# Optimization experiments

Hardware: AMD Instinct MI355X
Metric: run time of the kernel (lower is better)

Reference implementation:

```python
import jax, jax.numpy as jnp
import numpy as np

EPS = 1e-5
D_MODEL, N_HEADS, D_FF, SEQ, BATCH, THETA = 1024, 16, 4096, 2048, 4, 10000.0


def rmsnorm(x, g):
    rms = jnp.sqrt(jnp.mean(jnp.square(x), axis=-1, keepdims=True) + EPS)
    return (x / rms) * g


def rope(x, pos, theta):
    # x: [B, H, S, Dh]; pos: [S]
    dh = x.shape[-1]
    inv_freq = theta ** (-jnp.arange(0, dh, 2, dtype=x.dtype) / dh)  # [Dh/2]
    ang = pos.astype(x.dtype)[:, None] * inv_freq                    # [S, Dh/2]
    cos, sin = jnp.cos(ang), jnp.sin(ang)
    x1, x2 = x[..., ::2], x[..., 1::2]
    r1 = x1 * cos - x2 * sin
    r2 = x1 * sin + x2 * cos
    return jnp.stack([r1, r2], axis=-1).reshape(x.shape)


def setup_inputs() -> dict:
    key = jax.random.key(0)
    ks = jax.random.split(key, 10)
    s = 0.02
    return {
        "x": jax.random.normal(ks[0], (BATCH, SEQ, D_MODEL), jnp.float32),
        "token_positions": jnp.arange(SEQ, dtype=jnp.int64 if jax.config.x64_enabled else jnp.int32),
        "g1": jnp.ones((D_MODEL,), jnp.float32),
        "g2": jnp.ones((D_MODEL,), jnp.float32),
        "wq": jax.random.normal(ks[1], (D_MODEL, D_MODEL), jnp.float32) * s,
        "wk": jax.random.normal(ks[2], (D_MODEL, D_MODEL), jnp.float32) * s,
        "wv": jax.random.normal(ks[3], (D_MODEL, D_MODEL), jnp.float32) * s,
        "wo": jax.random.normal(ks[4], (D_MODEL, D_MODEL), jnp.float32) * s,
        "w1": jax.random.normal(ks[5], (D_MODEL, D_FF), jnp.float32) * s,
        "w2": jax.random.normal(ks[6], (D_FF, D_MODEL), jnp.float32) * s,
        "w3": jax.random.normal(ks[7], (D_MODEL, D_FF), jnp.float32) * s,
    }


def reference(x, token_positions, g1, g2, wq, wk, wv, wo, w1, w2, w3):
    B, S, D = x.shape
    H = N_HEADS
    Dh = D // H

    # --- RMSNorm 1 + causal RoPE self-attention ---
    h = rmsnorm(x, g1)
    q = (h @ wq).reshape(B, S, H, Dh).transpose(0, 2, 1, 3)  # [B,H,S,Dh]
    k = (h @ wk).reshape(B, S, H, Dh).transpose(0, 2, 1, 3)
    v = (h @ wv).reshape(B, S, H, Dh).transpose(0, 2, 1, 3)
    q = rope(q, token_positions, THETA)
    k = rope(k, token_positions, THETA)

    scores = jnp.einsum("bhqd,bhkd->bhqk", q, k) / jnp.sqrt(jnp.asarray(Dh, x.dtype))
    causal = jnp.tril(jnp.ones((S, S), bool))
    scores = jnp.where(causal, scores, jnp.asarray(-jnp.inf, x.dtype))
    attn = jax.nn.softmax(scores, axis=-1)
    ctx = jnp.einsum("bhqk,bhkd->bhqd", attn, v)             # [B,H,S,Dh]
    ctx = ctx.transpose(0, 2, 1, 3).reshape(B, S, D)
    attn_out = ctx @ wo

    y = x + attn_out  # residual

    # --- RMSNorm 2 + SwiGLU ---
    h2 = rmsnorm(y, g2)
    gate = jax.nn.silu(h2 @ w1) * (h2 @ w3)
    ff = gate @ w2

    return y + ff
```

## Files before the change

kernel.cpp:

```cpp
#include <hip/hip_runtime.h>
#include <hip/hip_bf16.h>
#include <cstdint>
#include <cstddef>

typedef __bf16 bf16_t;
typedef __bf16 bf16x8 __attribute__((ext_vector_type(8)));
typedef __bf16 bf16x4 __attribute__((ext_vector_type(4)));
typedef float  f32x4  __attribute__((ext_vector_type(4)));

#define D_MODEL 1024
#define SEQ     2048
#define NHEADS  16
#define DHEAD   64
#define DFF     4096

__device__ __forceinline__ void async_ld16(void* lds, const void* g) {
    __builtin_amdgcn_global_load_lds(
        (__attribute__((address_space(1))) void*)(void*)(g),
        (__attribute__((address_space(3))) void*)(lds), 16, 0, 0);
}

__device__ __forceinline__ void xcd_swizzle(int& bx, int& by) {
    const int gy = gridDim.y;
    const int i = blockIdx.x + gridDim.x * blockIdx.y;
    if ((gy & 7) == 0) {
        const int cy = gy >> 3;
        const int xcd = i & 7, j = i >> 3;
        bx = j / cy;
        by = xcd * cy + (j % cy);
    } else { bx = blockIdx.x; by = blockIdx.y; }
}

__global__ __launch_bounds__(256)
void transpose_cast_kernel(const float* __restrict__ src, bf16_t* __restrict__ dst,
                           int K, int N, int gstride, int goff)
{
    __shared__ float tile[32][33];
    const int bn = blockIdx.x * 32, bk = blockIdx.y * 32;
    const int tx = threadIdx.x & 31, ty = threadIdx.x >> 5;
#pragma unroll
    for (int i = 0; i < 32; i += 8)
        tile[ty + i][tx] = src[(size_t)(bk + ty + i) * N + bn + tx];
    __syncthreads();
#pragma unroll
    for (int i = 0; i < 32; i += 8) {
        const int n = bn + ty + i, kk = bk + tx;
        const int row = (n >> 4) * gstride + (n & 15) + goff;
        dst[(size_t)row * K + kk] = (bf16_t)tile[tx][ty + i];
    }
}

__global__ __launch_bounds__(256)
void transpose_v_kernel(const bf16_t* __restrict__ v, bf16_t* __restrict__ vt)
{
    __shared__ bf16_t T[64 * 66];
    const int bh = blockIdx.y, s0 = blockIdx.x * 64;
    const int tid = threadIdx.x;
    const size_t vb = (size_t)bh * SEQ * DHEAD;
#pragma unroll
    for (int h = 0; h < 2; ++h) {
        const int s = h * 32 + (tid >> 3), dc = (tid & 7) * 8;
        const bf16x8 vv = *(const bf16x8*)(v + vb + (size_t)(s0 + s) * DHEAD + dc);
#pragma unroll
        for (int j = 0; j < 8; ++j) T[(dc + j) * 66 + s] = vv[j];
    }
    __syncthreads();
    const size_t tb = (size_t)bh * DHEAD * SEQ;
    const uint32_t* Tw = (const uint32_t*)T;
#pragma unroll
    for (int h = 0; h < 2; ++h) {
        const int dh = h * 32 + (tid >> 3), kc = (tid & 7) * 8;
        uint4 o;
        o.x = Tw[dh * 33 + kc / 2 + 0];
        o.y = Tw[dh * 33 + kc / 2 + 1];
        o.z = Tw[dh * 33 + kc / 2 + 2];
        o.w = Tw[dh * 33 + kc / 2 + 3];
        *(uint4*)(vt + tb + (size_t)dh * SEQ + s0 + kc) = o;
    }
}

__global__ __launch_bounds__(256)
void rmsnorm_kernel(const float* __restrict__ x, const float* __restrict__ gw,
                    bf16_t* __restrict__ out)
{
    const int row = blockIdx.x, tid = threadIdx.x;
    const float4 v = ((const float4*)(x + (size_t)row * D_MODEL))[tid];
    float ss = v.x*v.x + v.y*v.y + v.z*v.z + v.w*v.w;
#pragma unroll
    for (int d = 1; d < 64; d <<= 1) ss += __shfl_xor(ss, d);
    __shared__ float red[4];
    if ((tid & 63) == 0) red[tid >> 6] = ss;
    __syncthreads();
    const float tot = red[0] + red[1] + red[2] + red[3];
    const float sc = rsqrtf(tot * (1.f / D_MODEL) + 1e-5f);
    const float4 gv = ((const float4*)gw)[tid];
    bf16x4 o;
    o[0] = (bf16_t)(v.x * sc * gv.x);
    o[1] = (bf16_t)(v.y * sc * gv.y);
    o[2] = (bf16_t)(v.z * sc * gv.z);
    o[3] = (bf16_t)(v.w * sc * gv.w);
    ((bf16x4*)(out + (size_t)row * D_MODEL))[tid] = o;
}

template <int MODE>
__global__ __launch_bounds__(512, 2)
void gemm256_kernel(const bf16_t* __restrict__ A, const bf16_t* __restrict__ Bt,
                    int M, int N, int K,
                    bf16_t* __restrict__ qo, bf16_t* __restrict__ ko, bf16_t* __restrict__ vo,
                    bf16_t* __restrict__ gate)
{
    __shared__ bf16x8 lds[8192];
    const int tid  = threadIdx.x;
    const int wave = tid >> 6;
    const int lane = tid & 63;
    const int r = lane & 15, g = lane >> 4;
    const int wm = wave >> 2;
    const int wn = wave & 3;
    const int r3 = (r >> 3) & 1;
    const int gx = g ^ (((r >> 2) & 1) << 1);
    const int cx0 = r3 * 4 + gx;
    const int cx1 = cx0 ^ 4;

    int bx, by;
    xcd_swizzle(bx, by);
    const int row0 = by * 256;
    const int col0 = bx * 256;

    const f32x4 fzero = {0.f, 0.f, 0.f, 0.f};
    f32x4 acc[8][4];
#pragma unroll
    for (int i = 0; i < 8; ++i)
#pragma unroll
        for (int j = 0; j < 4; ++j) acc[i][j] = fzero;

    const int kcx = ((tid & 7) ^ (((tid >> 5) & 1) << 1) ^ (((tid >> 6) & 1) << 2)) * 8;
    const bf16_t* aSrc = A  + (size_t)(row0 + (tid >> 3)) * K + kcx;
    const bf16_t* bSrc = Bt + (size_t)(col0 + (tid >> 3)) * K + kcx;

    const int aRB = wm * 1024 + r * 8;
    const int bRB = 2048 + (wn >> 1) * 1024 + ((wn & 1) * 64 + r) * 8;

#define STA(nb, ktn, h_, j_) \
    async_ld16(&lds[(nb) + (h_) * 1024 + (j_) * 512 + tid], \
               aSrc + (size_t)((h_) * 128 + (j_) * 64) * K + (ktn))
#define STB(nb, ktn, h_, j_) \
    async_ld16(&lds[(nb) + 2048 + (h_) * 1024 + (j_) * 512 + tid], \
               bSrc + (size_t)((h_) * 128 + (j_) * 64) * K + (ktn))

    STB(0, 0, 0, 0); STB(0, 0, 0, 1); STB(0, 0, 1, 0); STB(0, 0, 1, 1);
    STA(0, 0, 0, 0); STA(0, 0, 1, 0);
    STA(0, 0, 0, 1); STA(0, 0, 1, 1);
    asm volatile("s_waitcnt vmcnt(2)" ::: "memory");
    __builtin_amdgcn_s_barrier();

    bf16x8 aF[8], bF[8];

    const int NT = K >> 6;
    for (int t = 0; t < NT; ++t) {
        const int AB  = (t & 1) << 12;
        const int nb  = AB ^ 4096;
        const int ktn = (t + 1) << 6;
        const bool pf = (t + 1) < NT;

#pragma unroll
        for (int q = 0; q < 4; ++q) {
            aF[q * 2 + 0] = lds[AB + aRB + q * 128 + cx0];
            aF[q * 2 + 1] = lds[AB + aRB + q * 128 + cx1];
        }
#pragma unroll
        for (int n = 0; n < 2; ++n) {
            bF[n * 2 + 0] = lds[AB + bRB + n * 128 + cx0];
            bF[n * 2 + 1] = lds[AB + bRB + n * 128 + cx1];
        }
        if (pf) { STB(nb, ktn, 0, 0); STB(nb, ktn, 0, 1); }
        __builtin_amdgcn_s_barrier();
        asm volatile("s_waitcnt lgkmcnt(0)" ::: "memory");
        __builtin_amdgcn_sched_barrier(0);
        __builtin_amdgcn_s_setprio(1);
#pragma unroll
        for (int q = 0; q < 4; ++q)
#pragma unroll
            for (int n = 0; n < 2; ++n)
#pragma unroll
                for (int ks = 0; ks < 2; ++ks)
                    acc[q][n] = __builtin_amdgcn_mfma_f32_16x16x32_bf16(
                        aF[q * 2 + ks], bF[n * 2 + ks], acc[q][n], 0, 0, 0);
        __builtin_amdgcn_s_setprio(0);
        __builtin_amdgcn_s_barrier();

#pragma unroll
        for (int n = 0; n < 2; ++n) {
            bF[4 + n * 2 + 0] = lds[AB + bRB + (32 + n * 16) * 8 + cx0];
            bF[4 + n * 2 + 1] = lds[AB + bRB + (32 + n * 16) * 8 + cx1];
        }
        if (pf) { STB(nb, ktn, 1, 0); STB(nb, ktn, 1, 1); }
        __builtin_amdgcn_s_barrier();
        asm volatile("s_waitcnt lgkmcnt(0)" ::: "memory");
        __builtin_amdgcn_sched_barrier(0);
        __builtin_amdgcn_s_setprio(1);
#pragma unroll
        for (int q = 0; q < 4; ++q)
#pragma unroll
            for (int n = 0; n < 2; ++n)
#pragma unroll
                for (int ks = 0; ks < 2; ++ks)
                    acc[q][2 + n] = __builtin_amdgcn_mfma_f32_16x16x32_bf16(
                        aF[q * 2 + ks], bF[4 + n * 2 + ks], acc[q][2 + n], 0, 0, 0);
        __builtin_amdgcn_s_setprio(0);
        if (pf) asm volatile("s_waitcnt vmcnt(4)" ::: "memory");
        else    asm volatile("s_waitcnt vmcnt(0)" ::: "memory");
        __builtin_amdgcn_s_barrier();

#pragma unroll
        for (int q = 0; q < 4; ++q) {
            aF[q * 2 + 0] = lds[AB + aRB + (64 + q * 16) * 8 + cx0];
            aF[q * 2 + 1] = lds[AB + aRB + (64 + q * 16) * 8 + cx1];
        }
        if (pf) { STA(nb, ktn, 0, 0); STA(nb, ktn, 1, 0); }
        __builtin_amdgcn_s_barrier();
        asm volatile("s_waitcnt lgkmcnt(0)" ::: "memory");
        __builtin_amdgcn_sched_barrier(0);
        __builtin_amdgcn_s_setprio(1);
#pragma unroll
        for (int q = 0; q < 4; ++q)
#pragma unroll
            for (int n = 0; n < 2; ++n)
#pragma unroll
                for (int ks = 0; ks < 2; ++ks)
                    acc[4 + q][2 + n] = __builtin_amdgcn_mfma_f32_16x16x32_bf16(
                        aF[q * 2 + ks], bF[4 + n * 2 + ks], acc[4 + q][2 + n], 0, 0, 0);
        __builtin_amdgcn_s_setprio(0);
        __builtin_amdgcn_s_barrier();

        if (pf) { STA(nb, ktn, 0, 1); STA(nb, ktn, 1, 1); }
        __builtin_amdgcn_s_barrier();
        __builtin_amdgcn_s_setprio(1);
#pragma unroll
        for (int q = 0; q < 4; ++q)
#pragma unroll
            for (int n = 0; n < 2; ++n)
#pragma unroll
                for (int ks = 0; ks < 2; ++ks)
                    acc[4 + q][n] = __builtin_amdgcn_mfma_f32_16x16x32_bf16(
                        aF[q * 2 + ks], bF[n * 2 + ks], acc[4 + q][n], 0, 0, 0);
        __builtin_amdgcn_s_setprio(0);
        if (pf) asm volatile("s_waitcnt vmcnt(2)" ::: "memory");
        __builtin_amdgcn_s_barrier();
    }
#undef STA
#undef STB

    const int mbase = row0 + wm * 128 + g * 4;
    const int nbase = col0 + wn * 64 + r;

    if constexpr (MODE == 2) {
#pragma unroll
        for (int np = 0; np < 2; ++np) {
            const int gc = (col0 >> 1) + wn * 32 + np * 16 + r;
#pragma unroll
            for (int mt = 0; mt < 8; ++mt) {
#pragma unroll
                for (int e = 0; e < 4; ++e) {
                    const float v1 = acc[mt][2 * np][e];
                    const float v3 = acc[mt][2 * np + 1][e];
                    const float sv = v1 * __builtin_amdgcn_rcpf(1.f + __expf(-v1));
                    const int grow = mbase + mt * 16 + e;
                    gate[(size_t)grow * DFF + gc] = (bf16_t)(sv * v3);
                }
            }
        }
    } else {
#pragma unroll
        for (int nt = 0; nt < 4; ++nt) {
            const int gcol = nbase + nt * 16;
            const int mat  = gcol >> 10;
            const int d    = gcol & 1023;
            const int head = d >> 6;
            const int dh   = d & 63;
            const float invf = __expf((float)(dh & ~1) * -0.14391157f);
            const size_t hb = (size_t)head * SEQ * DHEAD + dh;
#pragma unroll
            for (int mt = 0; mt < 8; ++mt) {
#pragma unroll
                for (int e = 0; e < 4; ++e) {
                    const float val = acc[mt][nt][e];
                    const float partner = __shfl_xor(val, 1);
                    const int grow = mbase + mt * 16 + e;
                    const int b = grow >> 11;
                    const int s = grow & 2047;
                    const size_t dst = (size_t)b * NHEADS * SEQ * DHEAD + hb + (size_t)s * DHEAD;
                    if (mat == 2) {
                        vo[dst] = (bf16_t)val;
                    } else {
                        float sn, cs;
                        __sincosf((float)s * invf, &sn, &cs);
                        const float rv = (dh & 1) ? (partner * sn + val * cs)
                                                  : (val * cs - partner * sn);
                        if (mat == 0) qo[dst] = (bf16_t)(rv * 0.125f);
                        else          ko[dst] = (bf16_t)rv;
                    }
                }
            }
        }
    }
}

template <int MODE>
__global__ __launch_bounds__(256, 3)
void gemm128_kernel(const bf16_t* __restrict__ A, const bf16_t* __restrict__ Bt,
                    int M, int N, int K, const float* res, float* outf)
{
    __shared__ bf16x8 Al[1024];
    __shared__ bf16x8 Bl[1024];
    const int tid  = threadIdx.x;
    const int wave = tid >> 6;
    const int lane = tid & 63;
    const int r    = lane & 15;
    const int g    = lane >> 4;
    const int wm   = wave >> 1;
    const int wn   = wave & 1;
    const int r3 = (r >> 3) & 1;
    const int gx = g ^ (((r >> 2) & 1) << 1);
    const int cx0 = r3 * 4 + gx;
    const int cx1 = cx0 ^ 4;

    int bx, by;
    xcd_swizzle(bx, by);
    const int row0 = by * 128;
    const int col0 = bx * 128;

    const f32x4 fzero = {0.f, 0.f, 0.f, 0.f};
    f32x4 acc[4][4];
#pragma unroll
    for (int i = 0; i < 4; ++i)
#pragma unroll
        for (int j = 0; j < 4; ++j) acc[i][j] = fzero;

    const int kcx = ((tid & 7) ^ (((tid >> 5) & 1) << 1) ^ (((tid >> 6) & 1) << 2)) * 8;
    const bf16_t* a0 = A  + (size_t)(row0 + (tid >> 3)) * K + kcx;
    const bf16_t* b0 = Bt + (size_t)(col0 + (tid >> 3)) * K + kcx;

    for (int kt = 0; kt < K; kt += 64) {
#pragma unroll
        for (int j = 0; j < 4; ++j)
            async_ld16(&Al[j * 256 + tid], a0 + kt + (size_t)(j * 32) * K);
#pragma unroll
        for (int j = 0; j < 4; ++j)
            async_ld16(&Bl[j * 256 + tid], b0 + kt + (size_t)(j * 32) * K);
        __syncthreads();
#pragma unroll
        for (int s = 0; s < 2; ++s) {
            const int cx = s ? cx1 : cx0;
            bf16x8 af[4], bfr[4];
#pragma unroll
            for (int mt = 0; mt < 4; ++mt) af[mt]  = Al[(wm * 64 + mt * 16 + r) * 8 + cx];
#pragma unroll
            for (int nt = 0; nt < 4; ++nt) bfr[nt] = Bl[(wn * 64 + nt * 16 + r) * 8 + cx];
#pragma unroll
            for (int mt = 0; mt < 4; ++mt)
#pragma unroll
                for (int nt = 0; nt < 4; ++nt)
                    acc[mt][nt] = __builtin_amdgcn_mfma_f32_16x16x32_bf16(
                        af[mt], bfr[nt], acc[mt][nt], 0, 0, 0);
        }
        __syncthreads();
    }

    const int mbase = row0 + wm * 64 + g * 4;
    const int nbase = col0 + wn * 64 + r;
#pragma unroll
    for (int mt = 0; mt < 4; ++mt) {
#pragma unroll
        for (int nt = 0; nt < 4; ++nt) {
#pragma unroll
            for (int e = 0; e < 4; ++e) {
                const int grow = mbase + mt * 16 + e;
                const int gcol = nbase + nt * 16;
                const size_t idx = (size_t)grow * D_MODEL + gcol;
                outf[idx] = res[idx] + acc[mt][nt][e];
            }
        }
    }
}

__global__ __launch_bounds__(256)
void attn_kernel(const bf16_t* __restrict__ qg, const bf16_t* __restrict__ kg,
                 const bf16_t* __restrict__ vT, bf16_t* __restrict__ ctx)
{
    __shared__ bf16x8 lds[4096];
    const int qblk = (gridDim.x - 1) - blockIdx.x;
    const int bh   = blockIdx.y;
    const int tid  = threadIdx.x;
    const int wave = tid >> 6;
    const int lane = tid & 63;
    const int r = lane & 15, g = lane >> 4;
    const size_t base = (size_t)bh * SEQ * DHEAD;
    const int qw = qblk * 128 + wave * 32;

    bf16x8 qf[2][2];
#pragma unroll
    for (int rt = 0; rt < 2; ++rt)
#pragma unroll
        for (int kh = 0; kh < 2; ++kh)
            qf[rt][kh] = *(const bf16x8*)(qg + base + (size_t)(qw + rt*16 + r) * DHEAD + kh*32 + g*8);

    const f32x4 fzero = {0.f, 0.f, 0.f, 0.f};
    f32x4 O[2][4];
    float mi[2][4], li[2][4];
#pragma unroll
    for (int rt = 0; rt < 2; ++rt)
#pragma unroll
        for (int e = 0; e < 4; ++e) { mi[rt][e] = -1e30f; li[rt][e] = 0.f; }
#pragma unroll
    for (int rt = 0; rt < 2; ++rt)
#pragma unroll
        for (int d = 0; d < 4; ++d) O[rt][d] = fzero;

    bf16_t* const Pb = (bf16_t*)&lds[2048 + wave * 512];

    for (int kb = 0; kb <= qblk; ++kb) {
        const int k0 = kb * 128;
        {
            const int ghalf = (wave >> 1);
            const int key   = (wave & 1) * 64 + lane;
            const bf16_t* kp = kg + base + (size_t)(k0 + key) * DHEAD + ghalf * 8;
#pragma unroll
            for (int i = 0; i < 4; ++i)
                async_ld16(&lds[i * 256 + wave * 64], kp + i * 16);
        }
        {
            const bf16_t* vp = vT + base + (size_t)lane * SEQ + k0 + wave * 8;
#pragma unroll
            for (int i = 0; i < 4; ++i)
                async_ld16(&lds[1024 + i * 256 + wave * 64], vp + i * 32);
        }
        __syncthreads();

        f32x4 sc[2][8];
        __builtin_amdgcn_s_setprio(1);
#pragma unroll
        for (int ct = 0; ct < 8; ++ct) {
            const bf16x8 kf0 = lds[g * 128 + ct * 16 + r];
            const bf16x8 kf1 = lds[(4 + g) * 128 + ct * 16 + r];
            sc[0][ct] = __builtin_amdgcn_mfma_f32_16x16x32_bf16(qf[0][0], kf0, fzero, 0, 0, 0);
            sc[0][ct] = __builtin_amdgcn_mfma_f32_16x16x32_bf16(qf[0][1], kf1, sc[0][ct], 0, 0, 0);
            sc[1][ct] = __builtin_amdgcn_mfma_f32_16x16x32_bf16(qf[1][0], kf0, fzero, 0, 0, 0);
            sc[1][ct] = __builtin_amdgcn_mfma_f32_16x16x32_bf16(qf[1][1], kf1, sc[1][ct], 0, 0, 0);
        }
        __builtin_amdgcn_s_setprio(0);
        if (kb == qblk) {
#pragma unroll
            for (int rt = 0; rt < 2; ++rt)
#pragma unroll
                for (int ct = 0; ct < 8; ++ct)
#pragma unroll
                    for (int e = 0; e < 4; ++e)
                        if (ct * 16 + r > wave * 32 + rt * 16 + g * 4 + e)
                            sc[rt][ct][e] = -1e30f;
        }
#pragma unroll
        for (int rt = 0; rt < 2; ++rt) {
#pragma unroll
            for (int e = 0; e < 4; ++e) {
                float mx = sc[rt][0][e];
#pragma unroll
                for (int ct = 1; ct < 8; ++ct) mx = fmaxf(mx, sc[rt][ct][e]);
#pragma unroll
                for (int d = 1; d < 16; d <<= 1) mx = fmaxf(mx, __shfl_xor(mx, d));
                const float mnew  = fmaxf(mi[rt][e], mx);
                const float alpha = __expf(mi[rt][e] - mnew);
                mi[rt][e] = mnew;
                float pv[8], rs = 0.f;
#pragma unroll
                for (int ct = 0; ct < 8; ++ct) { pv[ct] = __expf(sc[rt][ct][e] - mnew); rs += pv[ct]; }
#pragma unroll
                for (int d = 1; d < 16; d <<= 1) rs += __shfl_xor(rs, d);
                li[rt][e] = li[rt][e] * alpha + rs;
#pragma unroll
                for (int dht = 0; dht < 4; ++dht) O[rt][dht][e] *= alpha;
                const int qlocal = rt * 16 + g * 4 + e;
#pragma unroll
                for (int ct = 0; ct < 8; ++ct) {
                    const int kchunk = ct * 2 + (r >> 3);
                    Pb[(kchunk * 32 + qlocal) * 8 + (r & 7)] = (bf16_t)pv[ct];
                }
            }
        }
        __builtin_amdgcn_s_setprio(1);
#pragma unroll
        for (int kt = 0; kt < 4; ++kt) {
            const bf16x8 pf0 = lds[2048 + wave * 512 + (kt * 4 + g) * 32 + r];
            const bf16x8 pf1 = lds[2048 + wave * 512 + (kt * 4 + g) * 32 + 16 + r];
#pragma unroll
            for (int dht = 0; dht < 4; ++dht) {
                const bf16x8 vf = lds[1024 + (kt * 4 + g) * 64 + dht * 16 + r];
                O[0][dht] = __builtin_amdgcn_mfma_f32_16x16x32_bf16(pf0, vf, O[0][dht], 0, 0, 0);
                O[1][dht] = __builtin_amdgcn_mfma_f32_16x16x32_bf16(pf1, vf, O[1][dht], 0, 0, 0);
            }
        }
        __builtin_amdgcn_s_setprio(0);
        __syncthreads();
    }

    const int b = bh >> 4, head = bh & 15;
#pragma unroll
    for (int rt = 0; rt < 2; ++rt) {
#pragma unroll
        for (int e = 0; e < 4; ++e) {
            const float inv = __builtin_amdgcn_rcpf(li[rt][e]);
            const int s = qw + rt * 16 + g * 4 + e;
            bf16_t* op = ctx + ((size_t)(b * SEQ + s)) * D_MODEL + head * DHEAD + r;
#pragma unroll
            for (int dht = 0; dht < 4; ++dht)
                op[dht * 16] = (bf16_t)(O[rt][dht][e] * inv);
        }
    }
}

extern "C" void kernel_launch(void* const* d_in, const int* in_sizes, int n_in,
                              void* d_out, int out_size, void* d_ws, size_t ws_size,
                              hipStream_t stream)
{
    (void)in_sizes; (void)n_in; (void)out_size; (void)ws_size;
    const float* x  = (const float*)d_in[0];
    const float* g1 = (const float*)d_in[2];
    const float* g2 = (const float*)d_in[3];
    const float* wq = (const float*)d_in[4];
    const float* wk = (const float*)d_in[5];
    const float* wv = (const float*)d_in[6];
    const float* wo = (const float*)d_in[7];
    const float* w1 = (const float*)d_in[8];
    const float* w2 = (const float*)d_in[9];
    const float* w3 = (const float*)d_in[10];
    float* out = (float*)d_out;
    char* ws = (char*)d_ws;
    const size_t MB = 1ull << 20;
    bf16_t* wqkvT = (bf16_t*)(ws + 0);
    bf16_t* woT   = (bf16_t*)(ws + 6  * MB);
    bf16_t* w13T  = (bf16_t*)(ws + 8  * MB);
    bf16_t* w2T   = (bf16_t*)(ws + 24 * MB);
    bf16_t* hbuf  = (bf16_t*)(ws + 32 * MB);
    bf16_t* qbuf  = (bf16_t*)(ws + 48 * MB);
    bf16_t* kbuf  = (bf16_t*)(ws + 64 * MB);
    bf16_t* vbuf  = (bf16_t*)(ws + 80 * MB);
    bf16_t* ctx   = (bf16_t*)(ws + 96 * MB);
    bf16_t* gate  = (bf16_t*)(ws + 48 * MB);
    bf16_t* vTb   = hbuf;

    dim3 blk(256);
    dim3 blk5(512);
    transpose_cast_kernel<<<dim3(32, 32),  blk, 0, stream>>>(wq, wqkvT,             1024, 1024, 16, 0);
    transpose_cast_kernel<<<dim3(32, 32),  blk, 0, stream>>>(wk, wqkvT + 1024*1024, 1024, 1024, 16, 0);
    transpose_cast_kernel<<<dim3(32, 32),  blk, 0, stream>>>(wv, wqkvT + 2048*1024, 1024, 1024, 16, 0);
    transpose_cast_kernel<<<dim3(32, 32),  blk, 0, stream>>>(wo, woT,               1024, 1024, 16, 0);
    transpose_cast_kernel<<<dim3(128, 32), blk, 0, stream>>>(w1, w13T,              1024, 4096, 32, 0);
    transpose_cast_kernel<<<dim3(128, 32), blk, 0, stream>>>(w3, w13T,              1024, 4096, 32, 16);
    transpose_cast_kernel<<<dim3(32, 128), blk, 0, stream>>>(w2, w2T,               4096, 1024, 16, 0);

    rmsnorm_kernel<<<dim3(8192), blk, 0, stream>>>(x, g1, hbuf);

    gemm256_kernel<0><<<dim3(12, 32), blk5, 0, stream>>>(hbuf, wqkvT, 8192, 3072, 1024,
        qbuf, kbuf, vbuf, nullptr);

    transpose_v_kernel<<<dim3(32, 64), blk, 0, stream>>>(vbuf, vTb);

    attn_kernel<<<dim3(16, 64), blk, 0, stream>>>(qbuf, kbuf, vTb, ctx);

    gemm128_kernel<1><<<dim3(8, 64), blk, 0, stream>>>(ctx, woT, 8192, 1024, 1024, x, out);

    rmsnorm_kernel<<<dim3(8192), blk, 0, stream>>>(out, g2, hbuf);

    gemm256_kernel<2><<<dim3(32, 32), blk5, 0, stream>>>(hbuf, w13T, 8192, 8192, 1024,
        nullptr, nullptr, nullptr, gate);

    gemm128_kernel<3><<<dim3(8, 64), blk, 0, stream>>>(gate, w2T, 8192, 1024, 4096, out, out);
}
```

Baseline: 687.8 us.

## Shrink attention key tile to 64, tile V transpose layout, skip masked waves

The attention kernel now walks keys in 64-wide tiles instead of 128, halving LDS use and declaring an occupancy target of 4 blocks per CU. The V-transpose kernel writes V^T in 8-key chunked tiles so each key block loads contiguously. Waves whose query rows lie entirely before the key tile skip the MFMA and softmax work, and the P buffer uses an XOR-swizzled layout to avoid LDS bank conflicts. The trade-off is twice as many loop iterations and barriers per block, while the smaller working set aims at more resident blocks and less wasted causal work.

```diff
diff --git a/kernel.cpp b/kernel.cpp
--- a/kernel.cpp
+++ b/kernel.cpp
@@ -75,7 +75,7 @@
         o.y = Tw[dh * 33 + kc / 2 + 1];
         o.z = Tw[dh * 33 + kc / 2 + 2];
         o.w = Tw[dh * 33 + kc / 2 + 3];
-        *(uint4*)(vt + tb + (size_t)dh * SEQ + s0 + kc) = o;
+        *(uint4*)(vt + tb + (size_t)((s0 + kc) >> 3) * 512 + dh * 8) = o;
     }
 }
 
@@ -383,11 +383,11 @@
     }
 }
 
-__global__ __launch_bounds__(256)
+__global__ __launch_bounds__(256, 4)
 void attn_kernel(const bf16_t* __restrict__ qg, const bf16_t* __restrict__ kg,
                  const bf16_t* __restrict__ vT, bf16_t* __restrict__ ctx)
 {
-    __shared__ bf16x8 lds[4096];
+    __shared__ bf16x8 lds[2048];
     const int qblk = (gridDim.x - 1) - blockIdx.x;
     const int bh   = blockIdx.y;
     const int tid  = threadIdx.x;
@@ -416,89 +416,87 @@
 #pragma unroll
         for (int d = 0; d < 4; ++d) O[rt][d] = fzero;
 
-    bf16_t* const Pb = (bf16_t*)&lds[2048 + wave * 512];
-
-    for (int kb = 0; kb <= qblk; ++kb) {
-        const int k0 = kb * 128;
+    bf16_t* const Pb = (bf16_t*)&lds[1024 + wave * 256];
+    const int pcx = ((r >> 2) & 3) << 1;
+
+    const int NKB = 2 * qblk + 2;
+    for (int kb = 0; kb < NKB; ++kb) {
+        const int k0 = kb * 64;
         {
-            const int ghalf = (wave >> 1);
-            const int key   = (wave & 1) * 64 + lane;
-            const bf16_t* kp = kg + base + (size_t)(k0 + key) * DHEAD + ghalf * 8;
-#pragma unroll
-            for (int i = 0; i < 4; ++i)
-                async_ld16(&lds[i * 256 + wave * 64], kp + i * 16);
+            const bf16_t* kp = kg + base + (size_t)(k0 + lane) * DHEAD + wave * 8;
+            async_ld16(&lds[tid], kp);
+            async_ld16(&lds[256 + tid], kp + 32);
         }
         {
-            const bf16_t* vp = vT + base + (size_t)lane * SEQ + k0 + wave * 8;
-#pragma unroll
-            for (int i = 0; i < 4; ++i)
-                async_ld16(&lds[1024 + i * 256 + wave * 64], vp + i * 32);
+            const bf16_t* vp = vT + base + (size_t)k0 * DHEAD + tid * 8;
+            async_ld16(&lds[512 + tid], vp);
+            async_ld16(&lds[768 + tid], vp + 2048);
         }
         __syncthreads();
 
-        f32x4 sc[2][8];
-        __builtin_amdgcn_s_setprio(1);
-#pragma unroll
-        for (int ct = 0; ct < 8; ++ct) {
-            const bf16x8 kf0 = lds[g * 128 + ct * 16 + r];
-            const bf16x8 kf1 = lds[(4 + g) * 128 + ct * 16 + r];
-            sc[0][ct] = __builtin_amdgcn_mfma_f32_16x16x32_bf16(qf[0][0], kf0, fzero, 0, 0, 0);
-            sc[0][ct] = __builtin_amdgcn_mfma_f32_16x16x32_bf16(qf[0][1], kf1, sc[0][ct], 0, 0, 0);
-            sc[1][ct] = __builtin_amdgcn_mfma_f32_16x16x32_bf16(qf[1][0], kf0, fzero, 0, 0, 0);
-            sc[1][ct] = __builtin_amdgcn_mfma_f32_16x16x32_bf16(qf[1][1], kf1, sc[1][ct], 0, 0, 0);
-        }
-        __builtin_amdgcn_s_setprio(0);
-        if (kb == qblk) {
-#pragma unroll
-            for (int rt = 0; rt < 2; ++rt)
-#pragma unroll
-                for (int ct = 0; ct < 8; ++ct)
-#pragma unroll
-                    for (int e = 0; e < 4; ++e)
-                        if (ct * 16 + r > wave * 32 + rt * 16 + g * 4 + e)
-                            sc[rt][ct][e] = -1e30f;
-        }
-#pragma unroll
-        for (int rt = 0; rt < 2; ++rt) {
-#pragma unroll
-            for (int e = 0; e < 4; ++e) {
-                float mx = sc[rt][0][e];
-#pragma unroll
-                for (int ct = 1; ct < 8; ++ct) mx = fmaxf(mx, sc[rt][ct][e]);
-#pragma unroll
-                for (int d = 1; d < 16; d <<= 1) mx = fmaxf(mx, __shfl_xor(mx, d));
-                const float mnew  = fmaxf(mi[rt][e], mx);
-                const float alpha = __expf(mi[rt][e] - mnew);
-                mi[rt][e] = mnew;
-                float pv[8], rs = 0.f;
-#pragma unroll
-                for (int ct = 0; ct < 8; ++ct) { pv[ct] = __expf(sc[rt][ct][e] - mnew); rs += pv[ct]; }
-#pragma unroll
-                for (int d = 1; d < 16; d <<= 1) rs += __shfl_xor(rs, d);
-                li[rt][e] = li[rt][e] * alpha + rs;
-#pragma unroll
-                for (int dht = 0; dht < 4; ++dht) O[rt][dht][e] *= alpha;
-                const int qlocal = rt * 16 + g * 4 + e;
-#pragma unroll
-                for (int ct = 0; ct < 8; ++ct) {
-                    const int kchunk = ct * 2 + (r >> 3);
-                    Pb[(kchunk * 32 + qlocal) * 8 + (r & 7)] = (bf16_t)pv[ct];
+        if (k0 <= qw + 31) {
+            f32x4 sc[2][4];
+            __builtin_amdgcn_s_setprio(1);
+#pragma unroll
+            for (int ct = 0; ct < 4; ++ct) {
+                const bf16x8 kf0 = lds[g * 64 + ct * 16 + r];
+                const bf16x8 kf1 = lds[(4 + g) * 64 + ct * 16 + r];
+                sc[0][ct] = __builtin_amdgcn_mfma_f32_16x16x32_bf16(qf[0][0], kf0, fzero, 0, 0, 0);
+                sc[0][ct] = __builtin_amdgcn_mfma_f32_16x16x32_bf16(qf[0][1], kf1, sc[0][ct], 0, 0, 0);
+                sc[1][ct] = __builtin_amdgcn_mfma_f32_16x16x32_bf16(qf[1][0], kf0, fzero, 0, 0, 0);
+                sc[1][ct] = __builtin_amdgcn_mfma_f32_16x16x32_bf16(qf[1][1], kf1, sc[1][ct], 0, 0, 0);
+            }
+            __builtin_amdgcn_s_setprio(0);
+            if (k0 + 63 > qw) {
+#pragma unroll
+                for (int rt = 0; rt < 2; ++rt)
+#pragma unroll
+                    for (int ct = 0; ct < 4; ++ct)
+#pragma unroll
+                        for (int e = 0; e < 4; ++e)
+                            if (k0 + ct * 16 + r > qw + rt * 16 + g * 4 + e)
+                                sc[rt][ct][e] = -1e30f;
+            }
+#pragma unroll
+            for (int rt = 0; rt < 2; ++rt) {
+#pragma unroll
+                for (int e = 0; e < 4; ++e) {
+                    float mx = fmaxf(fmaxf(sc[rt][0][e], sc[rt][1][e]),
+                                     fmaxf(sc[rt][2][e], sc[rt][3][e]));
+#pragma unroll
+                    for (int d = 1; d < 16; d <<= 1) mx = fmaxf(mx, __shfl_xor(mx, d));
+                    const float mnew  = fmaxf(mi[rt][e], mx);
+                    const float alpha = __expf(mi[rt][e] - mnew);
+                    mi[rt][e] = mnew;
+                    float pv[4], rs = 0.f;
+#pragma unroll
+                    for (int ct = 0; ct < 4; ++ct) { pv[ct] = __expf(sc[rt][ct][e] - mnew); rs += pv[ct]; }
+#pragma unroll
+                    for (int d = 1; d < 16; d <<= 1) rs += __shfl_xor(rs, d);
+                    li[rt][e] = li[rt][e] * alpha + rs;
+#pragma unroll
+                    for (int dht = 0; dht < 4; ++dht) O[rt][dht][e] *= alpha;
+                    const int qlocal = rt * 16 + g * 4 + e;
+#pragma unroll
+                    for (int ct = 0; ct < 4; ++ct)
+                        Pb[qlocal * 64 + ((ct * 16 + r) ^ (g << 4))] = (bf16_t)pv[ct];
                 }
             }
-        }
-        __builtin_amdgcn_s_setprio(1);
-#pragma unroll
-        for (int kt = 0; kt < 4; ++kt) {
-            const bf16x8 pf0 = lds[2048 + wave * 512 + (kt * 4 + g) * 32 + r];
-            const bf16x8 pf1 = lds[2048 + wave * 512 + (kt * 4 + g) * 32 + 16 + r];
-#pragma unroll
-            for (int dht = 0; dht < 4; ++dht) {
-                const bf16x8 vf = lds[1024 + (kt * 4 + g) * 64 + dht * 16 + r];
-                O[0][dht] = __builtin_amdgcn_mfma_f32_16x16x32_bf16(pf0, vf, O[0][dht], 0, 0, 0);
-                O[1][dht] = __builtin_amdgcn_mfma_f32_16x16x32_bf16(pf1, vf, O[1][dht], 0, 0, 0);
-            }
-        }
-        __builtin_amdgcn_s_setprio(0);
+            __builtin_amdgcn_s_setprio(1);
+#pragma unroll
+            for (int kt = 0; kt < 2; ++kt) {
+                const int cix = (kt * 4 + g) ^ pcx;
+                const bf16x8 pf0 = lds[1024 + wave * 256 + r * 8 + cix];
+                const bf16x8 pf1 = lds[1024 + wave * 256 + 128 + r * 8 + cix];
+#pragma unroll
+                for (int dht = 0; dht < 4; ++dht) {
+                    const bf16x8 vf = lds[512 + (kt * 4 + g) * 64 + dht * 16 + r];
+                    O[0][dht] = __builtin_amdgcn_mfma_f32_16x16x32_bf16(pf0, vf, O[0][dht], 0, 0, 0);
+                    O[1][dht] = __builtin_amdgcn_mfma_f32_16x16x32_bf16(pf1, vf, O[1][dht], 0, 0, 0);
+                }
+            }
+            __builtin_amdgcn_s_setprio(0);
+        }
         __syncthreads();
     }
 
```

After: 699.2 us. No clear change (+1.7%).
